# Kernel tuning notes

Measured on AMD Instinct MI355X. Metric: run time of the kernel, lower is better.

## Reference

```python
import jax, jax.numpy as jnp
import numpy as np

# candidate init bones from the original module
INIT_BONES = np.array([0, 1, 2, 4, 5, 6, 11, 12, 13, 16, 17, 18, 19, 20], dtype=np.int32)
SOFTMAX_TEMP = 20.0
DIST_THRESH = 0.1
NEG_INF = -1e4


def setup_inputs() -> dict:
    key = jax.random.key(0)
    k1, k2, k3 = jax.random.split(key, 3)
    B, N, J = 1, 65536, 25
    D, H, W = 32, 128, 128  # d = res // z_ratio, h = w = res
    x = jax.random.uniform(k1, (B, N, 3), jnp.float32, -0.9, 0.9)
    # bone transforms ~ identity + noise, valid homogeneous last row
    tfs = jnp.eye(4, dtype=jnp.float32)[None, None] + 0.05 * jax.random.normal(k2, (B, J, 4, 4), jnp.float32)
    tfs = tfs.at[:, :, 3, :].set(jnp.array([0.0, 0.0, 0.0, 1.0], jnp.float32))
    lbs_voxel = 0.1 * jax.random.normal(k3, (1, J, D, H, W), jnp.float32)
    init_bones = jnp.asarray(INIT_BONES)
    return {"x": x, "tfs": tfs, "lbs_voxel": lbs_voxel, "init_bones": init_bones}


def trilinear_sample(vox, coords):
    """vox: [J,D,H,W]; coords: [...,3] in [-1,1], x->W, y->H, z->D.
    align_corners=True, border padding. Returns [..., J]."""
    J, D, H, W = vox.shape
    cx = jnp.clip((coords[..., 0] + 1.0) * 0.5 * (W - 1), 0.0, W - 1)
    cy = jnp.clip((coords[..., 1] + 1.0) * 0.5 * (H - 1), 0.0, H - 1)
    cz = jnp.clip((coords[..., 2] + 1.0) * 0.5 * (D - 1), 0.0, D - 1)
    x0 = jnp.floor(cx).astype(jnp.int32); x1 = jnp.minimum(x0 + 1, W - 1)
    y0 = jnp.floor(cy).astype(jnp.int32); y1 = jnp.minimum(y0 + 1, H - 1)
    z0 = jnp.floor(cz).astype(jnp.int32); z1 = jnp.minimum(z0 + 1, D - 1)
    fx = cx - x0; fy = cy - y0; fz = cz - z0
    vf = vox.reshape(J, -1)

    def gather(zi, yi, xi):
        idx = (zi * H + yi) * W + xi
        return jnp.moveaxis(jnp.take(vf, idx, axis=1), 0, -1)  # [..., J]

    fx = fx[..., None]; fy = fy[..., None]; fz = fz[..., None]
    c00 = gather(z0, y0, x0) * (1 - fx) + gather(z0, y0, x1) * fx
    c01 = gather(z0, y1, x0) * (1 - fx) + gather(z0, y1, x1) * fx
    c10 = gather(z1, y0, x0) * (1 - fx) + gather(z1, y0, x1) * fx
    c11 = gather(z1, y1, x0) * (1 - fx) + gather(z1, y1, x1) * fx
    c0 = c00 * (1 - fy) + c01 * fy
    c1 = c10 * (1 - fy) + c11 * fy
    return c0 * (1 - fz) + c1 * fz


def reference(x, tfs, lbs_voxel, init_bones):
    """Voxel skinning query + multi-init candidate warp + argmax aggregation (agg).
    x: [B,N,3] deformed points; tfs: [B,J,4,4]; lbs_voxel: [1,J,D,H,W]; init_bones: [I]."""
    B, N, _ = x.shape
    xh = jnp.concatenate([x, jnp.ones_like(x[..., :1])], axis=-1)  # [B,N,4]
    # multi-init candidates: invert each init bone transform
    Ti = tfs[:, init_bones]                       # [B,I,4,4]
    Tinv = jnp.linalg.inv(Ti)
    xc = jnp.einsum('bipq,bnq->bnip', Tinv, xh)[..., :3]  # [B,N,I,3] canonical candidates
    # skinning weights: trilinear voxel query + tempered softmax over bones
    w = trilinear_sample(lbs_voxel[0], xc)        # [B,N,I,J]
    w = jax.nn.softmax(SOFTMAX_TEMP * w, axis=-1)
    # fused forward LBS: x_warp = sum_j w_j * (T_j @ x_cano)
    xc_h = jnp.concatenate([xc, jnp.ones_like(xc[..., :1])], axis=-1)  # [B,N,I,4]
    Txc = jnp.einsum('bjpq,bniq->bnijp', tfs[:, :, :3, :], xc_h)        # [B,N,I,J,3]
    x_warp = jnp.einsum('bnij,bnijp->bnip', w, Txc)                     # [B,N,I,3]
    # root-finding residual -> density per candidate, invalid candidates masked out
    err = jnp.linalg.norm(x_warp - x[:, :, None, :], axis=-1)  # [B,N,I]
    mask = err < DIST_THRESH
    density = jnp.where(mask, -err, NEG_INF)[..., None]        # [B,N,I,1]
    features = w[..., :15]                                     # [B,N,I,15]
    # agg(): argmax over candidate dim I, gather features/warp/mask at winner
    idx = jnp.argmax(density[..., 0], axis=-1)                 # [B,N]
    d_agg = jnp.max(density, axis=-2)                          # [B,N,1]
    f_agg = jnp.take_along_axis(features, idx[..., None, None], axis=-2)[..., 0, :]  # [B,N,15]
    w_agg = jnp.take_along_axis(xc, idx[..., None, None], axis=-2)[..., 0, :]        # [B,N,3]
    m_agg = jnp.take_along_axis(mask, idx[..., None], axis=-1)[..., 0]               # [B,N]
    return d_agg, f_agg, m_agg, w_agg
```

## Files before the change

### kernel.cpp

```cpp
#include <hip/hip_runtime.h>
#include <math.h>

#define NJ 25
#define NJP 32
#define VD 32
#define VH 128
#define VW 128
#define TEMP 20.0f
#define NEGINF (-10000.0f)
#define DHW (VD*VH*VW)
#define NCELL 4096
#define TINV_FLOATS 256


__device__ __forceinline__ int cell_of(float v) {
    int c = (int)((v + 1.0f) * 8.0f);
    return min(max(c, 0), 15);
}
__device__ __forceinline__ int morton12(int ix, int iy, int iz) {
    int m = 0;
    #pragma unroll
    for (int b = 0; b < 4; ++b)
        m |= (((ix>>b)&1)<<(3*b)) | (((iy>>b)&1)<<(3*b+1)) | (((iz>>b)&1)<<(3*b+2));
    return m;
}

__global__ void setup_kernel(const float* __restrict__ tfs,
                             const int* __restrict__ bones,
                             float* __restrict__ tinv,
                             int* __restrict__ hist, int ni) {
    int b = blockIdx.x, t = threadIdx.x;
    if (b == 0) {
        if (t >= ni) return;
        const float* T = tfs + (size_t)bones[t] * 16;
        double r00=T[0], r01=T[1], r02=T[2],  tx=T[3];
        double r10=T[4], r11=T[5], r12=T[6],  ty=T[7];
        double r20=T[8], r21=T[9], r22=T[10], tz=T[11];
        double c00 = r11*r22 - r12*r21;
        double c01 = r12*r20 - r10*r22;
        double c02 = r10*r21 - r11*r20;
        double det = r00*c00 + r01*c01 + r02*c02;
        double id  = 1.0/det;
        double i00 = c00*id;
        double i01 = (r02*r21 - r01*r22)*id;
        double i02 = (r01*r12 - r02*r11)*id;
        double i10 = c01*id;
        double i11 = (r00*r22 - r02*r20)*id;
        double i12 = (r02*r10 - r00*r12)*id;
        double i20 = c02*id;
        double i21 = (r01*r20 - r00*r21)*id;
        double i22 = (r00*r11 - r01*r10)*id;
        double itx = -(i00*tx + i01*ty + i02*tz);
        double ity = -(i10*tx + i11*ty + i12*tz);
        double itz = -(i20*tx + i21*ty + i22*tz);
        float* o = tinv + t*12;
        o[0]=(float)i00; o[1]=(float)i01; o[2] =(float)i02; o[3] =(float)itx;
        o[4]=(float)i10; o[5]=(float)i11; o[6] =(float)i12; o[7] =(float)ity;
        o[8]=(float)i20; o[9]=(float)i21; o[10]=(float)i22; o[11]=(float)itz;
    } else if (hist != nullptr) {
        int g = (b-1)*256 + t;
        if (g < NCELL) hist[g] = 0;
    }
}

__global__ __launch_bounds__(256) void transpose_vox_kernel(const float* __restrict__ vox,
                                                            float* __restrict__ vt,
                                                            const float* __restrict__ x,
                                                            int* __restrict__ hist, int N) {
    __shared__ float lds[NJ*129];
    int row = blockIdx.x;
    int t = threadIdx.x;
    const float4* v4 = (const float4*)vox;
    for (int idx = t; idx < NJ*32; idx += 256) {
        int j  = idx >> 5;
        int x4 = idx & 31;
        float4 v = v4[(size_t)j*(DHW/4) + (size_t)row*32 + x4];
        float* l = &lds[j*129 + x4*4];
        l[0]=v.x; l[1]=v.y; l[2]=v.z; l[3]=v.w;
    }
    __syncthreads();
    float4* out4 = (float4*)(vt + (size_t)row * (VW*NJP));
    for (int idx = t; idx < (VW*NJP)/4; idx += 256) {
        int xx = idx >> 3;
        int jq = (idx & 7) * 4;
        float4 o;
        o.x = (jq+0 < NJ) ? lds[(jq+0)*129 + xx] : 0.0f;
        o.y = (jq+1 < NJ) ? lds[(jq+1)*129 + xx] : 0.0f;
        o.z = (jq+2 < NJ) ? lds[(jq+2)*129 + xx] : 0.0f;
        o.w = (jq+3 < NJ) ? lds[(jq+3)*129 + xx] : 0.0f;
        out4[idx] = o;
    }
    for (int g = blockIdx.x*256 + t; g < N; g += gridDim.x*256) {
        int m = morton12(cell_of(x[g*3+0]), cell_of(x[g*3+1]), cell_of(x[g*3+2]));
        atomicAdd(&hist[m], 1);
    }
}

__global__ __launch_bounds__(1024) void scan_kernel(const int* __restrict__ hist,
                                                    int* __restrict__ offs) {
    __shared__ int part[1024];
    int t = threadIdx.x;
    int4 h = ((const int4*)hist)[t];
    int s = h.x + h.y + h.z + h.w;
    part[t] = s;
    __syncthreads();
    for (int off = 1; off < 1024; off <<= 1) {
        int v = (t >= off) ? part[t-off] : 0;
        __syncthreads();
        part[t] += v;
        __syncthreads();
    }
    int excl = part[t] - s;
    offs[4*t+0] = excl;
    offs[4*t+1] = excl + h.x;
    offs[4*t+2] = excl + h.x + h.y;
    offs[4*t+3] = excl + h.x + h.y + h.z;
}
__global__ void scatter_kernel(const float* __restrict__ x, int* __restrict__ offs,
                               int* __restrict__ perm, int N) {
    int g = blockIdx.x*256 + threadIdx.x;
    if (g >= N) return;
    int m = morton12(cell_of(x[g*3+0]), cell_of(x[g*3+1]), cell_of(x[g*3+2]));
    int pos = atomicAdd(&offs[m], 1);
    perm[pos] = g;
}

template<bool VT>
__global__ __launch_bounds__(256) void deformer_cp_kernel(
        const float* __restrict__ x,
        const float* __restrict__ tfs,
        const float* __restrict__ vsrc,
        const float* __restrict__ tinv,
        const int* __restrict__ perm,
        float* __restrict__ out, int N, int ni) {
    int t = threadIdx.x;
    int j = t & 31;

    int nwg = gridDim.x;
    int q = nwg >> 3, r = nwg & 7;
    int xcd = blockIdx.x & 7, blk = blockIdx.x >> 3;
    int lb = (xcd < r ? xcd*(q+1) : r*(q+1) + (xcd-r)*q) + blk;

    int ns = lb*8 + (t >> 5);
    if (ns >= N) return;
    int n = perm ? perm[ns] : ns;

    float px = x[n*3+0], py = x[n*3+1], pz = x[n*3+2];

    int jj = (j < NJ) ? j : (NJ-1);
    const float* Mj = tfs + jj*16;
    float m0=Mj[0], m1=Mj[1], m2 =Mj[2],  m3 =Mj[3];
    float m4=Mj[4], m5=Mj[5], m6 =Mj[6],  m7 =Mj[7];
    float m8=Mj[8], m9=Mj[9], m10=Mj[10], m11=Mj[11];
    bool chv = (j < NJ);

    float bestD = -3.0e38f; int bestIdx = 0;
    float bestEv = 0.0f, bestInvs = 1.0f;

    #pragma unroll 1
    for (int i = 0; i < ni; ++i) {
        const float* Ti = &tinv[i*12];
        float cx = Ti[0]*px + Ti[1]*py + Ti[2] *pz + Ti[3];
        float cy = Ti[4]*px + Ti[5]*py + Ti[6] *pz + Ti[7];
        float cz = Ti[8]*px + Ti[9]*py + Ti[10]*pz + Ti[11];

        float gx = fminf(fmaxf((cx + 1.0f) * (0.5f*(VW-1)), 0.0f), (float)(VW-1));
        float gy = fminf(fmaxf((cy + 1.0f) * (0.5f*(VH-1)), 0.0f), (float)(VH-1));
        float gz = fminf(fmaxf((cz + 1.0f) * (0.5f*(VD-1)), 0.0f), (float)(VD-1));
        int x0 = (int)gx, y0 = (int)gy, z0 = (int)gz;
        int x1 = min(x0+1, VW-1), y1 = min(y0+1, VH-1), z1 = min(z0+1, VD-1);
        float fx = gx - (float)x0, fy = gy - (float)y0, fz = gz - (float)z0;
        float ax = 1.0f - fx, ay = 1.0f - fy, az = 1.0f - fz;
        float w000 = ax*ay*az, w001 = fx*ay*az, w010 = ax*fy*az, w011 = fx*fy*az;
        float w100 = ax*ay*fz, w101 = fx*ay*fz, w110 = ax*fy*fz, w111 = fx*fy*fz;

        float v000,v001,v010,v011,v100,v101,v110,v111;
        if (VT) {
            int o   = ((z0*VH + y0)*VW + x0)*NJP + j;
            int dz  = (z1 - z0) * (VH*VW*NJP);
            int dy  = (y1 - y0) * (VW*NJP);
            int dxo = (x1 - x0) * NJP;
            v000 = vsrc[o];          v001 = vsrc[o+dxo];
            v010 = vsrc[o+dy];       v011 = vsrc[o+dy+dxo];
            v100 = vsrc[o+dz];       v101 = vsrc[o+dz+dxo];
            v110 = vsrc[o+dz+dy];    v111 = vsrc[o+dz+dy+dxo];
        } else {
            int o   = jj*DHW + (z0*VH + y0)*VW + x0;
            int dz  = (z1 - z0) * (VH*VW);
            int dy  = (y1 - y0) * VW;
            int dxo = (x1 - x0);
            v000 = vsrc[o];          v001 = vsrc[o+dxo];
            v010 = vsrc[o+dy];       v011 = vsrc[o+dy+dxo];
            v100 = vsrc[o+dz];       v101 = vsrc[o+dz+dxo];
            v110 = vsrc[o+dz+dy];    v111 = vsrc[o+dz+dy+dxo];
        }
        float v = v000*w000 + v001*w001 + v010*w010 + v011*w011
                + v100*w100 + v101*w101 + v110*w110 + v111*w111;

        float ev = chv ? __expf(TEMP * v) : 0.0f;
        float mx = m0*cx + m1*cy + m2 *cz + m3;
        float my_= m4*cx + m5*cy + m6 *cz + m7;
        float mz = m8*cx + m9*cy + m10*cz + m11;

        float rs = ev, rx = ev*mx, ry = ev*my_, rz = ev*mz;
        #pragma unroll
        for (int mk = 1; mk < 32; mk <<= 1) {
            rs += __shfl_xor(rs, mk, 32);
            rx += __shfl_xor(rx, mk, 32);
            ry += __shfl_xor(ry, mk, 32);
            rz += __shfl_xor(rz, mk, 32);
        }
        float invs = 1.0f / rs;
        float dxp = rx*invs - px, dyp = ry*invs - py, dzp = rz*invs - pz;
        float err = sqrtf(dxp*dxp + dyp*dyp + dzp*dzp);
        float d = (err < 0.1f) ? -err : NEGINF;

        if (d > bestD) {
            bestD = d; bestIdx = i; bestEv = ev; bestInvs = invs;
        }
    }

    float* o_d = out;
    float* o_f = out + N;
    float* o_m = out + (size_t)N*16;
    float* o_w = out + (size_t)N*17;
    if (j < 15) {
        o_f[(size_t)n*15 + j] = bestEv * bestInvs;
    } else if (j == 15) {
        o_d[n] = bestD;
    } else if (j == 16) {
        o_m[n] = (bestD > -9999.0f) ? 1.0f : 0.0f;
    } else if (j < 20) {
        int rr = j - 17;
        const float* Tr = &tinv[bestIdx*12 + rr*4];
        o_w[(size_t)n*3 + rr] = Tr[0]*px + Tr[1]*py + Tr[2]*pz + Tr[3];
    }
}

extern "C" void kernel_launch(void* const* d_in, const int* in_sizes, int n_in,
                              void* d_out, int out_size, void* d_ws, size_t ws_size,
                              hipStream_t stream) {
    const float* x     = (const float*)d_in[0];
    const float* tfs   = (const float*)d_in[1];
    const float* vox   = (const float*)d_in[2];
    const int*   bones = (const int*)  d_in[3];
    int N  = in_sizes[0] / 3;
    int ni = in_sizes[3];

    float* ws = (float*)d_ws;
    size_t vt_off    = (size_t)TINV_FLOATS + NCELL*2 + (size_t)N;
    size_t vt_floats = (size_t)DHW * NJP;
    size_t need_all  = vt_off + vt_floats;

    float* tinv = ws;
    int*   hist = (int*)(ws + TINV_FLOATS);
    int*   offs = hist + NCELL;
    int*   perm = offs + NCELL;
    float* vt   = ws + vt_off;

    bool useVT = ws_size >= need_all * sizeof(float);
    int nblk = (N + 7) / 8;

    if (useVT) {
        hipLaunchKernelGGL(setup_kernel, dim3(1 + NCELL/256), dim3(256), 0, stream,
                           tfs, bones, tinv, hist, ni);
        hipLaunchKernelGGL(transpose_vox_kernel, dim3(VD*VH), dim3(256), 0, stream,
                           vox, vt, x, hist, N);
        hipLaunchKernelGGL(scan_kernel, dim3(1), dim3(1024), 0, stream, hist, offs);
        hipLaunchKernelGGL(scatter_kernel, dim3((N+255)/256), dim3(256), 0, stream,
                           x, offs, perm, N);
        hipLaunchKernelGGL((deformer_cp_kernel<true>), dim3(nblk), dim3(256), 0, stream,
                           x, tfs, vt, tinv, perm, (float*)d_out, N, ni);
    } else {
        hipLaunchKernelGGL(setup_kernel, dim3(1), dim3(64), 0, stream,
                           tfs, bones, tinv, (int*)nullptr, ni);
        hipLaunchKernelGGL((deformer_cp_kernel<false>), dim3(nblk), dim3(256), 0, stream,
                           x, tfs, vox, tinv, (const int*)nullptr,
                           (float*)d_out, N, ni);
    }
}
```

Baseline: 229.7 us.

## Process four joints per lane with float4 voxel loads, eight lanes per point

Each point is now handled by 8 lanes instead of 32, and each lane covers 4 joints using float4 loads from the joint-padded transposed voxel grid. The per-candidate shuffle reduction shrinks from 5 steps to 3, and each wavefront covers four times as many points. This is meant to cut per-point instruction count, shuffle cost and scalar load overhead. In exchange it raises register use (48 matrix floats per lane plus the float4 loads), which may lower occupancy.

Result: faster. 212.0 us (-7.7%).

```diff
diff --git a/kernel.cpp b/kernel.cpp
--- a/kernel.cpp
+++ b/kernel.cpp
@@ -126,7 +126,7 @@
 }
 
 template<bool VT>
-__global__ __launch_bounds__(256) void deformer_cp_kernel(
+__global__ __launch_bounds__(256) void deformer_cp8_kernel(
         const float* __restrict__ x,
         const float* __restrict__ tfs,
         const float* __restrict__ vsrc,
@@ -134,28 +134,31 @@
         const int* __restrict__ perm,
         float* __restrict__ out, int N, int ni) {
     int t = threadIdx.x;
-    int j = t & 31;
+    int l = t & 7;
 
     int nwg = gridDim.x;
     int q = nwg >> 3, r = nwg & 7;
     int xcd = blockIdx.x & 7, blk = blockIdx.x >> 3;
     int lb = (xcd < r ? xcd*(q+1) : r*(q+1) + (xcd-r)*q) + blk;
 
-    int ns = lb*8 + (t >> 5);
+    int ns = lb*32 + (t >> 3);
     if (ns >= N) return;
     int n = perm ? perm[ns] : ns;
 
     float px = x[n*3+0], py = x[n*3+1], pz = x[n*3+2];
 
-    int jj = (j < NJ) ? j : (NJ-1);
-    const float* Mj = tfs + jj*16;
-    float m0=Mj[0], m1=Mj[1], m2 =Mj[2],  m3 =Mj[3];
-    float m4=Mj[4], m5=Mj[5], m6 =Mj[6],  m7 =Mj[7];
-    float m8=Mj[8], m9=Mj[9], m10=Mj[10], m11=Mj[11];
-    bool chv = (j < NJ);
-
-    float bestD = -3.0e38f; int bestIdx = 0;
-    float bestEv = 0.0f, bestInvs = 1.0f;
+    int c0 = l*4;
+    float M[4][12];
+    #pragma unroll
+    for (int cc = 0; cc < 4; ++cc) {
+        const float* Mj = tfs + min(c0+cc, NJ-1)*16;
+        #pragma unroll
+        for (int r2 = 0; r2 < 12; ++r2) M[cc][r2] = Mj[r2];
+    }
+    bool v0 = (c0+0 < NJ), v1 = (c0+1 < NJ), v2 = (c0+2 < NJ), v3 = (c0+3 < NJ);
+
+    float bestD = -3.0e38f; int bestIdx = 0; float bestInvs = 1.0f;
+    float bE0 = 0.f, bE1 = 0.f, bE2 = 0.f, bE3 = 0.f;
 
     #pragma unroll 1
     for (int i = 0; i < ni; ++i) {
@@ -174,41 +177,73 @@
         float w000 = ax*ay*az, w001 = fx*ay*az, w010 = ax*fy*az, w011 = fx*fy*az;
         float w100 = ax*ay*fz, w101 = fx*ay*fz, w110 = ax*fy*fz, w111 = fx*fy*fz;
 
-        float v000,v001,v010,v011,v100,v101,v110,v111;
+        float vv0, vv1, vv2, vv3;
         if (VT) {
-            int o   = ((z0*VH + y0)*VW + x0)*NJP + j;
+            int o   = ((z0*VH + y0)*VW + x0)*NJP + c0;
             int dz  = (z1 - z0) * (VH*VW*NJP);
             int dy  = (y1 - y0) * (VW*NJP);
             int dxo = (x1 - x0) * NJP;
-            v000 = vsrc[o];          v001 = vsrc[o+dxo];
-            v010 = vsrc[o+dy];       v011 = vsrc[o+dy+dxo];
-            v100 = vsrc[o+dz];       v101 = vsrc[o+dz+dxo];
-            v110 = vsrc[o+dz+dy];    v111 = vsrc[o+dz+dy+dxo];
+            float4 a000 = *(const float4*)&vsrc[o];
+            float4 a001 = *(const float4*)&vsrc[o+dxo];
+            float4 a010 = *(const float4*)&vsrc[o+dy];
+            float4 a011 = *(const float4*)&vsrc[o+dy+dxo];
+            float4 a100 = *(const float4*)&vsrc[o+dz];
+            float4 a101 = *(const float4*)&vsrc[o+dz+dxo];
+            float4 a110 = *(const float4*)&vsrc[o+dz+dy];
+            float4 a111 = *(const float4*)&vsrc[o+dz+dy+dxo];
+            vv0 = a000.x*w000 + a001.x*w001 + a010.x*w010 + a011.x*w011
+                + a100.x*w100 + a101.x*w101 + a110.x*w110 + a111.x*w111;
+            vv1 = a000.y*w000 + a001.y*w001 + a010.y*w010 + a011.y*w011
+                + a100.y*w100 + a101.y*w101 + a110.y*w110 + a111.y*w111;
+            vv2 = a000.z*w000 + a001.z*w001 + a010.z*w010 + a011.z*w011
+                + a100.z*w100 + a101.z*w101 + a110.z*w110 + a111.z*w111;
+            vv3 = a000.w*w000 + a001.w*w001 + a010.w*w010 + a011.w*w011
+                + a100.w*w100 + a101.w*w101 + a110.w*w110 + a111.w*w111;
         } else {
-            int o   = jj*DHW + (z0*VH + y0)*VW + x0;
+            int cell = (z0*VH + y0)*VW + x0;
             int dz  = (z1 - z0) * (VH*VW);
             int dy  = (y1 - y0) * VW;
             int dxo = (x1 - x0);
-            v000 = vsrc[o];          v001 = vsrc[o+dxo];
-            v010 = vsrc[o+dy];       v011 = vsrc[o+dy+dxo];
-            v100 = vsrc[o+dz];       v101 = vsrc[o+dz+dxo];
-            v110 = vsrc[o+dz+dy];    v111 = vsrc[o+dz+dy+dxo];
+            float vvs[4];
+            #pragma unroll
+            for (int cc = 0; cc < 4; ++cc) {
+                const float* vj = vsrc + (size_t)min(c0+cc, NJ-1)*DHW + cell;
+                vvs[cc] = vj[0]*w000       + vj[dxo]*w001
+                        + vj[dy]*w010      + vj[dy+dxo]*w011
+                        + vj[dz]*w100      + vj[dz+dxo]*w101
+                        + vj[dz+dy]*w110   + vj[dz+dy+dxo]*w111;
+            }
+            vv0 = vvs[0]; vv1 = vvs[1]; vv2 = vvs[2]; vv3 = vvs[3];
         }
-        float v = v000*w000 + v001*w001 + v010*w010 + v011*w011
-                + v100*w100 + v101*w101 + v110*w110 + v111*w111;
-
-        float ev = chv ? __expf(TEMP * v) : 0.0f;
-        float mx = m0*cx + m1*cy + m2 *cz + m3;
-        float my_= m4*cx + m5*cy + m6 *cz + m7;
-        float mz = m8*cx + m9*cy + m10*cz + m11;
-
-        float rs = ev, rx = ev*mx, ry = ev*my_, rz = ev*mz;
+
+        float ev0 = v0 ? __expf(TEMP * vv0) : 0.0f;
+        float ev1 = v1 ? __expf(TEMP * vv1) : 0.0f;
+        float ev2 = v2 ? __expf(TEMP * vv2) : 0.0f;
+        float ev3 = v3 ? __expf(TEMP * vv3) : 0.0f;
+
+        float rs = (ev0 + ev1) + (ev2 + ev3);
+        float mx0 = M[0][0]*cx + M[0][1]*cy + M[0][2] *cz + M[0][3];
+        float my0 = M[0][4]*cx + M[0][5]*cy + M[0][6] *cz + M[0][7];
+        float mz0 = M[0][8]*cx + M[0][9]*cy + M[0][10]*cz + M[0][11];
+        float mx1 = M[1][0]*cx + M[1][1]*cy + M[1][2] *cz + M[1][3];
+        float my1 = M[1][4]*cx + M[1][5]*cy + M[1][6] *cz + M[1][7];
+        float mz1 = M[1][8]*cx + M[1][9]*cy + M[1][10]*cz + M[1][11];
+        float mx2 = M[2][0]*cx + M[2][1]*cy + M[2][2] *cz + M[2][3];
+        float my2 = M[2][4]*cx + M[2][5]*cy + M[2][6] *cz + M[2][7];
+        float mz2 = M[2][8]*cx + M[2][9]*cy + M[2][10]*cz + M[2][11];
+        float mx3 = M[3][0]*cx + M[3][1]*cy + M[3][2] *cz + M[3][3];
+        float my3 = M[3][4]*cx + M[3][5]*cy + M[3][6] *cz + M[3][7];
+        float mz3 = M[3][8]*cx + M[3][9]*cy + M[3][10]*cz + M[3][11];
+        float rx = ev0*mx0 + ev1*mx1 + ev2*mx2 + ev3*mx3;
+        float ry = ev0*my0 + ev1*my1 + ev2*my2 + ev3*my3;
+        float rz = ev0*mz0 + ev1*mz1 + ev2*mz2 + ev3*mz3;
+
         #pragma unroll
-        for (int mk = 1; mk < 32; mk <<= 1) {
-            rs += __shfl_xor(rs, mk, 32);
-            rx += __shfl_xor(rx, mk, 32);
-            ry += __shfl_xor(ry, mk, 32);
-            rz += __shfl_xor(rz, mk, 32);
+        for (int mk = 1; mk < 8; mk <<= 1) {
+            rs += __shfl_xor(rs, mk, 8);
+            rx += __shfl_xor(rx, mk, 8);
+            ry += __shfl_xor(ry, mk, 8);
+            rz += __shfl_xor(rz, mk, 8);
         }
         float invs = 1.0f / rs;
         float dxp = rx*invs - px, dyp = ry*invs - py, dzp = rz*invs - pz;
@@ -216,7 +251,8 @@
         float d = (err < 0.1f) ? -err : NEGINF;
 
         if (d > bestD) {
-            bestD = d; bestIdx = i; bestEv = ev; bestInvs = invs;
+            bestD = d; bestIdx = i; bestInvs = invs;
+            bE0 = ev0; bE1 = ev1; bE2 = ev2; bE3 = ev3;
         }
     }
 
@@ -224,14 +260,19 @@
     float* o_f = out + N;
     float* o_m = out + (size_t)N*16;
     float* o_w = out + (size_t)N*17;
-    if (j < 15) {
-        o_f[(size_t)n*15 + j] = bestEv * bestInvs;
-    } else if (j == 15) {
+    if (l < 4) {
+        int kb = c0;
+        float e0 = bE0*bestInvs, e1 = bE1*bestInvs, e2 = bE2*bestInvs, e3 = bE3*bestInvs;
+        float* of = &o_f[(size_t)n*15 + kb];
+        if (kb+0 < 15) of[0] = e0;
+        if (kb+1 < 15) of[1] = e1;
+        if (kb+2 < 15) of[2] = e2;
+        if (kb+3 < 15) of[3] = e3;
+    } else if (l == 4) {
         o_d[n] = bestD;
-    } else if (j == 16) {
         o_m[n] = (bestD > -9999.0f) ? 1.0f : 0.0f;
-    } else if (j < 20) {
-        int rr = j - 17;
+    } else {
+        int rr = l - 5;
         const float* Tr = &tinv[bestIdx*12 + rr*4];
         o_w[(size_t)n*3 + rr] = Tr[0]*px + Tr[1]*py + Tr[2]*pz + Tr[3];
     }
@@ -259,7 +300,7 @@
     float* vt   = ws + vt_off;
 
     bool useVT = ws_size >= need_all * sizeof(float);
-    int nblk = (N + 7) / 8;
+    int nblk = (N + 31) / 32;
 
     if (useVT) {
         hipLaunchKernelGGL(setup_kernel, dim3(1 + NCELL/256), dim3(256), 0, stream,
@@ -269,12 +310,12 @@
         hipLaunchKernelGGL(scan_kernel, dim3(1), dim3(1024), 0, stream, hist, offs);
         hipLaunchKernelGGL(scatter_kernel, dim3((N+255)/256), dim3(256), 0, stream,
                            x, offs, perm, N);
-        hipLaunchKernelGGL((deformer_cp_kernel<true>), dim3(nblk), dim3(256), 0, stream,
+        hipLaunchKernelGGL((deformer_cp8_kernel<true>), dim3(nblk), dim3(256), 0, stream,
                            x, tfs, vt, tinv, perm, (float*)d_out, N, ni);
     } else {
         hipLaunchKernelGGL(setup_kernel, dim3(1), dim3(64), 0, stream,
                            tfs, bones, tinv, (int*)nullptr, ni);
-        hipLaunchKernelGGL((deformer_cp_kernel<false>), dim3(nblk), dim3(256), 0, stream,
+        hipLaunchKernelGGL((deformer_cp8_kernel<false>), dim3(nblk), dim3(256), 0, stream,
                            x, tfs, vox, tinv, (const int*)nullptr,
                            (float*)d_out, N, ni);
     }
```
